# Optimization experiments

Measured on AMD Instinct MI355X. Metric: run time of the kernel, lower is better.

The kernel has to match this reference:

```python
import jax, jax.numpy as jnp
import numpy as np

N = 256
IN_FEATURES = 2048
OUT_FEATURES = 128
KERNEL_DIMS = 32


def setup_inputs() -> dict:
    key = jax.random.key(0)
    kx, kt = jax.random.split(key)
    x = jax.random.normal(kx, (N, IN_FEATURES), dtype=jnp.float32)
    T = jax.random.normal(kt, (IN_FEATURES, OUT_FEATURES, KERNEL_DIMS), dtype=jnp.float32)
    return {"x": x, "T": T}


def reference(x, T):
    # matrices: [N, out_features, kernel_dims]
    matrices = (x @ T.reshape(IN_FEATURES, OUT_FEATURES * KERNEL_DIMS)).reshape(
        -1, OUT_FEATURES, KERNEL_DIMS
    )
    # pairwise L1 distance over kernel dims: [N, N, out_features]
    norm = jnp.abs(matrices[None, :, :, :] - matrices[:, None, :, :]).sum(axis=3)
    # o_b[j, f] = sum_i exp(-norm[i, j, f]); includes self term exp(0)=1, as in original
    o_b = jnp.exp(-norm).sum(axis=0)  # [N, out_features]
    # mean=False in this configuration, so no division by batch size
    return jnp.concatenate((x, o_b), axis=1)  # [N, in_features + out_features]
```

## Files before the change

kernel.cpp:

```cpp
#include <hip/hip_runtime.h>
#include <hip/hip_bf16.h>
#include <stdint.h>

#define IN_F 2048
#define OUT_F 128
#define KD 32
#define NR 256
#define OC 2176
#define OD 4096
#define THRESH 32.0f

typedef __bf16 bf16x8 __attribute__((ext_vector_type(8)));
typedef float  f32x4  __attribute__((ext_vector_type(4)));

__global__ __launch_bounds__(256) void tproj_kernel(const float* __restrict__ x,
                                                    const float* __restrict__ Tm,
                                                    float* __restrict__ out,
                                                    __bf16* __restrict__ xb2,
                                                    __bf16* __restrict__ Tb) {
    __shared__ __bf16 o4[4][64][8];

    const int bid = blockIdx.x;
    if (bid < 1024) {
        const int t  = threadIdx.x;
        const int kt = bid >> 4;
        const int fo = bid & 15;
        const int kl = t >> 3;
        const int fl = t & 7;
        const int f  = fo * 8 + fl;
        const int k  = kt * 32 + kl;

        float v[32];
        const float* src = Tm + (size_t)k * OD + f * KD;
        #pragma unroll
        for (int q = 0; q < 8; ++q) {
            f32x4 w = *reinterpret_cast<const f32x4*>(src + q * 4);
            v[q * 4]     = w[0];
            v[q * 4 + 1] = w[1];
            v[q * 4 + 2] = w[2];
            v[q * 4 + 3] = w[3];
        }

        float s1[16], d1[16];
        #pragma unroll
        for (int e = 0; e < 16; ++e) { s1[e] = v[2*e] + v[2*e+1]; d1[e] = v[2*e] - v[2*e+1]; }
        float s2[8], d2[8];
        #pragma unroll
        for (int e = 0; e < 8; ++e)  { s2[e] = s1[2*e] + s1[2*e+1]; d2[e] = s1[2*e] - s1[2*e+1]; }
        float s3[4], d3[4];
        #pragma unroll
        for (int e = 0; e < 4; ++e)  { s3[e] = s2[2*e] + s2[2*e+1]; d3[e] = s2[2*e] - s2[2*e+1]; }
        float s4[2], d4[2];
        #pragma unroll
        for (int e = 0; e < 2; ++e)  { s4[e] = s3[2*e] + s3[2*e+1]; d4[e] = s3[2*e] - s3[2*e+1]; }
        const float s5 = s4[0] + s4[1];
        const float d5 = s4[0] - s4[1];

        float pr[8];
        pr[0] = s5;
        { float s = 0.f;
          #pragma unroll
          for (int e = 0; e < 16; ++e) s += d1[e];
          pr[1] = s; }
        { float s = 0.f;
          #pragma unroll
          for (int e = 0; e < 8; ++e) s += d2[e];
          pr[2] = s; }
        pr[3] = (d3[0] + d3[1]) + (d3[2] + d3[3]);
        pr[4] = d4[0] + d4[1];
        pr[5] = d5;
        { float s = 0.f;
          #pragma unroll
          for (int g = 0; g < 8; ++g) s += d1[2*g] - d1[2*g+1];
          pr[6] = s; }
        pr[7] = s3[0] - s3[1] - s3[2] + s3[3];

        const int li0 = ((kl >> 3) & 3) * 16 + (fl & 1) * 8;
        #pragma unroll
        for (int p = 0; p < 8; ++p)
            o4[fl >> 1][li0 + p][kl & 7] = (__bf16)pr[p];
        __syncthreads();

        const int cl = t >> 6, l = t & 63;
        const size_t c0 = (size_t)kt * 64 + fo * 4;
        *reinterpret_cast<bf16x8*>(Tb + (c0 + cl) * 512 + l * 8) =
            *reinterpret_cast<const bf16x8*>(&o4[cl][l][0]);
    } else {
        const int q   = (bid - 1024) * 256 + threadIdx.x;
        const int row = q & 255;
        const int k0  = (q >> 8) << 3;
        const float* src = &x[row * IN_F + k0];
        float4 v0 = *reinterpret_cast<const float4*>(src);
        float4 v1 = *reinterpret_cast<const float4*>(src + 4);
        *reinterpret_cast<float4*>(&out[row * OC + k0])     = v0;
        *reinterpret_cast<float4*>(&out[row * OC + k0 + 4]) = v1;
        bf16x8 p = { (__bf16)v0.x, (__bf16)v0.y, (__bf16)v0.z, (__bf16)v0.w,
                     (__bf16)v1.x, (__bf16)v1.y, (__bf16)v1.z, (__bf16)v1.w };
        *reinterpret_cast<bf16x8*>(&xb2[(size_t)q * 8]) = p;
    }
}

struct SFrag { bf16x8 a, b0, b1; };

__device__ __forceinline__ SFrag s_load(const __bf16* __restrict__ xb2,
                                        const __bf16* __restrict__ Tb,
                                        int h, int n0fr, int ot0, int l) {
    SFrag s;
    s.a = *reinterpret_cast<const bf16x8*>(xb2 + ((size_t)(h * 4 + (l >> 4)) * 256 + n0fr) * 8);
    const __bf16* bb = Tb + (((size_t)h * 64 + ot0) * 64 + l) * 8;
    s.b0 = *reinterpret_cast<const bf16x8*>(bb);
    s.b1 = *reinterpret_cast<const bf16x8*>(bb + 512);
    return s;
}

__global__ __launch_bounds__(256, 4) void sgemm_kernel(const __bf16* __restrict__ xb2,
                                                       const __bf16* __restrict__ Tb,
                                                       float* __restrict__ Pp) {
    const int tid = threadIdx.x;
    const int l   = tid & 63;
    const int wid = tid >> 6;
    const int fr  = l & 15, fg = l >> 4;
    const int co  = blockIdx.x;
    const int bn  = blockIdx.y;
    const int ks  = blockIdx.z;
    const int ot0 = co * 2;
    const int n0  = bn * 64 + wid * 16;
    const int h0  = ks * 8;
    const int n0fr = n0 + fr;

    f32x4 acc0 = {}, acc1 = {};

#define CMP(s) do { \
        acc0 = __builtin_amdgcn_mfma_f32_16x16x32_bf16((s).a, (s).b0, acc0, 0, 0, 0); \
        acc1 = __builtin_amdgcn_mfma_f32_16x16x32_bf16((s).a, (s).b1, acc1, 0, 0, 0); \
    } while (0)

    SFrag s0 = s_load(xb2, Tb, h0 + 0, n0fr, ot0, l);
    SFrag s1 = s_load(xb2, Tb, h0 + 1, n0fr, ot0, l);
    SFrag s2 = s_load(xb2, Tb, h0 + 2, n0fr, ot0, l);

    CMP(s0); s0 = s_load(xb2, Tb, h0 + 3, n0fr, ot0, l);
    CMP(s1); s1 = s_load(xb2, Tb, h0 + 4, n0fr, ot0, l);
    CMP(s2); s2 = s_load(xb2, Tb, h0 + 5, n0fr, ot0, l);
    CMP(s0); s0 = s_load(xb2, Tb, h0 + 6, n0fr, ot0, l);
    CMP(s1); s1 = s_load(xb2, Tb, h0 + 7, n0fr, ot0, l);
    CMP(s2);
    CMP(s0);
    CMP(s1);
#undef CMP

    float* dst = Pp + ((size_t)ks << 18);
    const int o0 = co * 32;
    const int nb = n0 + fg * 4;
    *reinterpret_cast<f32x4*>(&dst[(size_t)(o0 + fr)      * NR + nb]) = acc0;
    *reinterpret_cast<f32x4*>(&dst[(size_t)(o0 + 16 + fr) * NR + nb]) = acc1;
}

__global__ __launch_bounds__(256, 2) void screen_kernel(const float* __restrict__ Pp,
                                                        const float* __restrict__ x,
                                                        const float* __restrict__ Tm,
                                                        float* __restrict__ out) {
    __shared__ float P8s[256][8];
    __shared__ float part[4][64];

    const int f    = blockIdx.x;
    const int jq   = blockIdx.y;
    const int tid  = threadIdx.x;
    const int lane = tid & 63;
    const int wid  = tid >> 6;
    const int j    = jq * 64 + lane;

    #pragma unroll
    for (int p = 0; p < 8; ++p) {
        float s = 0.f;
        #pragma unroll
        for (int ks = 0; ks < 8; ++ks)
            s += Pp[((size_t)ks << 18) + (size_t)(f * 8 + p) * NR + tid];
        P8s[tid][p] = s;
    }
    __syncthreads();

    const f32x4 qj0 = *reinterpret_cast<const f32x4*>(&P8s[j][0]);
    const f32x4 qj1 = *reinterpret_cast<const f32x4*>(&P8s[j][4]);

    float acc = 0.f;
    const int i0 = wid * 64;
    #pragma unroll 2
    for (int ii = 0; ii < 64; ++ii) {
        const int i = i0 + ii;
        f32x4 r0 = *reinterpret_cast<const f32x4*>(&P8s[i][0]);
        f32x4 r1 = *reinterpret_cast<const f32x4*>(&P8s[i][4]);
        f32x4 d0 = r0 - qj0;
        f32x4 d1 = r1 - qj1;
        float m0 = fmaxf(fmaxf(fabsf(d0[0]), fabsf(d0[1])), fabsf(d0[2]));
        float m1 = fmaxf(fmaxf(fabsf(d0[3]), fabsf(d1[0])), fabsf(d1[1]));
        float m2 = fmaxf(fabsf(d1[2]), fabsf(d1[3]));
        const float mx = fmaxf(fmaxf(m0, m1), m2);

        const bool ok = (mx < THRESH) && (i != j);
        if (__builtin_expect(__any(ok), 0)) {
            if (ok) {
                f32x4 ad[8] = {};
                const float* xi = x + (size_t)i * IN_F;
                const float* xj = x + (size_t)j * IN_F;
                for (int k = 0; k < IN_F; ++k) {
                    const float dk = xi[k] - xj[k];
                    const float* tr = Tm + (size_t)k * OD + f * KD;
                    #pragma unroll
                    for (int q = 0; q < 8; ++q) {
                        f32x4 tv = *reinterpret_cast<const f32x4*>(tr + q * 4);
                        ad[q] += dk * tv;
                    }
                }
                float norm = 0.f;
                #pragma unroll
                for (int q = 0; q < 8; ++q)
                    norm += fabsf(ad[q][0]) + fabsf(ad[q][1])
                          + fabsf(ad[q][2]) + fabsf(ad[q][3]);
                acc += __expf(-norm);
            }
        }
    }

    if (wid == jq) acc += 1.0f;

    part[wid][lane] = acc;
    __syncthreads();
    if (tid < 64) {
        float s = part[0][tid] + part[1][tid] + part[2][tid] + part[3][tid];
        out[(jq * 64 + tid) * OC + IN_F + f] = s;
    }
}

extern "C" void kernel_launch(void* const* d_in, const int* in_sizes, int n_in,
                              void* d_out, int out_size, void* d_ws, size_t ws_size,
                              hipStream_t stream) {
    const float* x  = (const float*)d_in[0];
    const float* Tm = (const float*)d_in[1];
    float* out = (float*)d_out;
    char*  ws  = (char*)d_ws;

    __bf16* Tb  = (__bf16*)ws;
    __bf16* xb2 = (__bf16*)(ws + (4u << 20));
    float*  Pp  = (float*)(ws + (5u << 20));

    tproj_kernel<<<dim3(1280), 256, 0, stream>>>(x, Tm, out, xb2, Tb);
    sgemm_kernel<<<dim3(32, 4, 8), 256, 0, stream>>>(xb2, Tb, Pp);
    screen_kernel<<<dim3(128, 4), 256, 0, stream>>>(Pp, x, Tm, out);
}
```

Before: 29.05 us.

## Fuse T projection and screening GEMM into one kernel with bf16 partials

Merges the T Hadamard-style projection kernel and the bf16 MFMA GEMM into a single kernel. Each block transforms a 128-row K slice of T into shared memory and streams x tiles through a double-buffered LDS stage, which removes the intermediate Tb/xb2 global round trip and one launch. Split-K grows from 8 to 16, and the partial sums are stored as bf16 to halve their traffic, with the screen kernel reducing the 16 partials using vector loads. The costs are extra precision loss in the screening projections and more partial slices to sum.

```diff
diff --git a/kernel.cpp b/kernel.cpp
--- a/kernel.cpp
+++ b/kernel.cpp
@@ -9,29 +9,52 @@
 #define OC 2176
 #define OD 4096
 #define THRESH 32.0f
+#define KSN 16
+#define OPN (1024 * 256)
 
 typedef __bf16 bf16x8 __attribute__((ext_vector_type(8)));
+typedef __bf16 bf16x4 __attribute__((ext_vector_type(4)));
 typedef float  f32x4  __attribute__((ext_vector_type(4)));
-
-__global__ __launch_bounds__(256) void tproj_kernel(const float* __restrict__ x,
-                                                    const float* __restrict__ Tm,
-                                                    float* __restrict__ out,
-                                                    __bf16* __restrict__ xb2,
-                                                    __bf16* __restrict__ Tb) {
-    __shared__ __bf16 o4[4][64][8];
-
-    const int bid = blockIdx.x;
-    if (bid < 1024) {
-        const int t  = threadIdx.x;
-        const int kt = bid >> 4;
-        const int fo = bid & 15;
-        const int kl = t >> 3;
-        const int fl = t & 7;
-        const int f  = fo * 8 + fl;
-        const int k  = kt * 32 + kl;
+typedef uint16_t u16x8 __attribute__((ext_vector_type(8)));
+
+__global__ __launch_bounds__(256, 2) void fused_kernel(const float* __restrict__ x,
+                                                       const float* __restrict__ Tm,
+                                                       float* __restrict__ out,
+                                                       __bf16* __restrict__ Pp) {
+    __shared__ __bf16 Bs[32][136];
+    __shared__ __bf16 As[2][4][256][8];
+
+    const int tid  = threadIdx.x;
+    const int lane = tid & 63;
+    const int wid  = tid >> 6;
+    const int fr   = lane & 15, fg = lane >> 4;
+    const int bid  = blockIdx.x;
+    const int ks   = bid & 15;
+    const int fo   = bid >> 4;
+    const int k0   = ks * 128;
+
+    {
+        const int row = bid >> 1;
+        const int off = (bid & 1) * 1024 + tid * 4;
+        float4 v = *reinterpret_cast<const float4*>(&x[row * IN_F + off]);
+        *reinterpret_cast<float4*>(&out[row * OC + off]) = v;
+    }
+
+    float4 xs[8];
+    const int kslot = tid & 7;
+    const int nrow8 = tid >> 3;
+    #pragma unroll
+    for (int p = 0; p < 8; ++p)
+        xs[p] = *reinterpret_cast<const float4*>(&x[(p * 32 + nrow8) * IN_F + k0 + kslot * 4]);
+
+    #pragma unroll 1
+    for (int r = 0; r < 2; ++r) {
+        const int idx = r * 256 + tid;
+        const int fl  = idx & 3;
+        const int kl  = idx >> 2;
+        const float* src = Tm + (size_t)(k0 + kl) * OD + (fo * 4 + fl) * KD;
 
         float v[32];
-        const float* src = Tm + (size_t)k * OD + f * KD;
         #pragma unroll
         for (int q = 0; q < 8; ++q) {
             f32x4 w = *reinterpret_cast<const f32x4*>(src + q * 4);
@@ -75,88 +98,67 @@
           pr[6] = s; }
         pr[7] = s3[0] - s3[1] - s3[2] + s3[3];
 
-        const int li0 = ((kl >> 3) & 3) * 16 + (fl & 1) * 8;
         #pragma unroll
         for (int p = 0; p < 8; ++p)
-            o4[fl >> 1][li0 + p][kl & 7] = (__bf16)pr[p];
-        __syncthreads();
-
-        const int cl = t >> 6, l = t & 63;
-        const size_t c0 = (size_t)kt * 64 + fo * 4;
-        *reinterpret_cast<bf16x8*>(Tb + (c0 + cl) * 512 + l * 8) =
-            *reinterpret_cast<const bf16x8*>(&o4[cl][l][0]);
-    } else {
-        const int q   = (bid - 1024) * 256 + threadIdx.x;
-        const int row = q & 255;
-        const int k0  = (q >> 8) << 3;
-        const float* src = &x[row * IN_F + k0];
-        float4 v0 = *reinterpret_cast<const float4*>(src);
-        float4 v1 = *reinterpret_cast<const float4*>(src + 4);
-        *reinterpret_cast<float4*>(&out[row * OC + k0])     = v0;
-        *reinterpret_cast<float4*>(&out[row * OC + k0 + 4]) = v1;
-        bf16x8 p = { (__bf16)v0.x, (__bf16)v0.y, (__bf16)v0.z, (__bf16)v0.w,
-                     (__bf16)v1.x, (__bf16)v1.y, (__bf16)v1.z, (__bf16)v1.w };
-        *reinterpret_cast<bf16x8*>(&xb2[(size_t)q * 8]) = p;
+            Bs[fl * 8 + p][kl] = (__bf16)pr[p];
+    }
+
+    #pragma unroll
+    for (int p = 0; p < 8; ++p) {
+        bf16x4 b = { (__bf16)xs[p].x, (__bf16)xs[p].y, (__bf16)xs[p].z, (__bf16)xs[p].w };
+        *reinterpret_cast<bf16x4*>(&As[0][kslot >> 1][p * 32 + nrow8][(kslot & 1) * 4]) = b;
+    }
+    __syncthreads();
+
+    f32x4 acc[4][2] = {};
+
+    #pragma unroll 1
+    for (int c = 0; c < 4; ++c) {
+        const int buf = c & 1;
+        if (c < 3) {
+            #pragma unroll
+            for (int p = 0; p < 8; ++p)
+                xs[p] = *reinterpret_cast<const float4*>(
+                    &x[(p * 32 + nrow8) * IN_F + k0 + (c + 1) * 32 + kslot * 4]);
+        }
+
+        bf16x8 bfrag[2];
+        #pragma unroll
+        for (int oi = 0; oi < 2; ++oi)
+            bfrag[oi] = *reinterpret_cast<const bf16x8*>(&Bs[oi * 16 + fr][c * 32 + fg * 8]);
+        #pragma unroll
+        for (int mi = 0; mi < 4; ++mi) {
+            bf16x8 af = *reinterpret_cast<const bf16x8*>(&As[buf][fg][wid * 64 + mi * 16 + fr][0]);
+            acc[mi][0] = __builtin_amdgcn_mfma_f32_16x16x32_bf16(af, bfrag[0], acc[mi][0], 0, 0, 0);
+            acc[mi][1] = __builtin_amdgcn_mfma_f32_16x16x32_bf16(af, bfrag[1], acc[mi][1], 0, 0, 0);
+        }
+
+        if (c < 3) {
+            __syncthreads();
+            #pragma unroll
+            for (int p = 0; p < 8; ++p) {
+                bf16x4 b = { (__bf16)xs[p].x, (__bf16)xs[p].y, (__bf16)xs[p].z, (__bf16)xs[p].w };
+                *reinterpret_cast<bf16x4*>(&As[buf ^ 1][kslot >> 1][p * 32 + nrow8][(kslot & 1) * 4]) = b;
+            }
+            __syncthreads();
+        }
+    }
+
+    __bf16* dst = Pp + (size_t)ks * OPN;
+    #pragma unroll
+    for (int mi = 0; mi < 4; ++mi) {
+        #pragma unroll
+        for (int oi = 0; oi < 2; ++oi) {
+            const int op = fo * 32 + oi * 16 + fr;
+            const int nb = wid * 64 + mi * 16 + fg * 4;
+            bf16x4 v = { (__bf16)acc[mi][oi][0], (__bf16)acc[mi][oi][1],
+                         (__bf16)acc[mi][oi][2], (__bf16)acc[mi][oi][3] };
+            *reinterpret_cast<bf16x4*>(&dst[(size_t)op * NR + nb]) = v;
+        }
     }
 }
 
-struct SFrag { bf16x8 a, b0, b1; };
-
-__device__ __forceinline__ SFrag s_load(const __bf16* __restrict__ xb2,
-                                        const __bf16* __restrict__ Tb,
-                                        int h, int n0fr, int ot0, int l) {
-    SFrag s;
-    s.a = *reinterpret_cast<const bf16x8*>(xb2 + ((size_t)(h * 4 + (l >> 4)) * 256 + n0fr) * 8);
-    const __bf16* bb = Tb + (((size_t)h * 64 + ot0) * 64 + l) * 8;
-    s.b0 = *reinterpret_cast<const bf16x8*>(bb);
-    s.b1 = *reinterpret_cast<const bf16x8*>(bb + 512);
-    return s;
-}
-
-__global__ __launch_bounds__(256, 4) void sgemm_kernel(const __bf16* __restrict__ xb2,
-                                                       const __bf16* __restrict__ Tb,
-                                                       float* __restrict__ Pp) {
-    const int tid = threadIdx.x;
-    const int l   = tid & 63;
-    const int wid = tid >> 6;
-    const int fr  = l & 15, fg = l >> 4;
-    const int co  = blockIdx.x;
-    const int bn  = blockIdx.y;
-    const int ks  = blockIdx.z;
-    const int ot0 = co * 2;
-    const int n0  = bn * 64 + wid * 16;
-    const int h0  = ks * 8;
-    const int n0fr = n0 + fr;
-
-    f32x4 acc0 = {}, acc1 = {};
-
-#define CMP(s) do { \
-        acc0 = __builtin_amdgcn_mfma_f32_16x16x32_bf16((s).a, (s).b0, acc0, 0, 0, 0); \
-        acc1 = __builtin_amdgcn_mfma_f32_16x16x32_bf16((s).a, (s).b1, acc1, 0, 0, 0); \
-    } while (0)
-
-    SFrag s0 = s_load(xb2, Tb, h0 + 0, n0fr, ot0, l);
-    SFrag s1 = s_load(xb2, Tb, h0 + 1, n0fr, ot0, l);
-    SFrag s2 = s_load(xb2, Tb, h0 + 2, n0fr, ot0, l);
-
-    CMP(s0); s0 = s_load(xb2, Tb, h0 + 3, n0fr, ot0, l);
-    CMP(s1); s1 = s_load(xb2, Tb, h0 + 4, n0fr, ot0, l);
-    CMP(s2); s2 = s_load(xb2, Tb, h0 + 5, n0fr, ot0, l);
-    CMP(s0); s0 = s_load(xb2, Tb, h0 + 6, n0fr, ot0, l);
-    CMP(s1); s1 = s_load(xb2, Tb, h0 + 7, n0fr, ot0, l);
-    CMP(s2);
-    CMP(s0);
-    CMP(s1);
-#undef CMP
-
-    float* dst = Pp + ((size_t)ks << 18);
-    const int o0 = co * 32;
-    const int nb = n0 + fg * 4;
-    *reinterpret_cast<f32x4*>(&dst[(size_t)(o0 + fr)      * NR + nb]) = acc0;
-    *reinterpret_cast<f32x4*>(&dst[(size_t)(o0 + 16 + fr) * NR + nb]) = acc1;
-}
-
-__global__ __launch_bounds__(256, 2) void screen_kernel(const float* __restrict__ Pp,
+__global__ __launch_bounds__(256, 2) void screen_kernel(const __bf16* __restrict__ Pp,
                                                         const float* __restrict__ x,
                                                         const float* __restrict__ Tm,
                                                         float* __restrict__ out) {
@@ -170,13 +172,22 @@
     const int wid  = tid >> 6;
     const int j    = jq * 64 + lane;
 
-    #pragma unroll
-    for (int p = 0; p < 8; ++p) {
-        float s = 0.f;
-        #pragma unroll
-        for (int ks = 0; ks < 8; ++ks)
-            s += Pp[((size_t)ks << 18) + (size_t)(f * 8 + p) * NR + tid];
-        P8s[tid][p] = s;
+    {
+        const int p  = tid >> 5;
+        const int n0 = (tid & 31) * 8;
+        const uint16_t* base = reinterpret_cast<const uint16_t*>(Pp)
+                             + (size_t)(f * 8 + p) * NR + n0;
+        float a[8] = {};
+        #pragma unroll
+        for (int ks = 0; ks < KSN; ++ks) {
+            u16x8 v = *reinterpret_cast<const u16x8*>(base + (size_t)ks * OPN);
+            #pragma unroll
+            for (int e = 0; e < 8; ++e)
+                a[e] += __builtin_bit_cast(float, (uint32_t)v[e] << 16);
+        }
+        #pragma unroll
+        for (int e = 0; e < 8; ++e)
+            P8s[n0 + e][p] = a[e];
     }
     __syncthreads();
 
@@ -238,13 +249,9 @@
     const float* x  = (const float*)d_in[0];
     const float* Tm = (const float*)d_in[1];
     float* out = (float*)d_out;
-    char*  ws  = (char*)d_ws;
-
-    __bf16* Tb  = (__bf16*)ws;
-    __bf16* xb2 = (__bf16*)(ws + (4u << 20));
-    float*  Pp  = (float*)(ws + (5u << 20));
-
-    tproj_kernel<<<dim3(1280), 256, 0, stream>>>(x, Tm, out, xb2, Tb);
-    sgemm_kernel<<<dim3(32, 4, 8), 256, 0, stream>>>(xb2, Tb, Pp);
+
+    __bf16* Pp = (__bf16*)d_ws;
+
+    fused_kernel<<<dim3(512), 256, 0, stream>>>(x, Tm, out, Pp);
     screen_kernel<<<dim3(128, 4), 256, 0, stream>>>(Pp, x, Tm, out);
 }
```

Result: faster. 28.48 us (-2.0%).
